# Kernel tuning notes

Hardware: AMD Instinct MI355X
Metric: run time of the kernel (lower is better)

The kernel has to match this reference:

```python
import jax, jax.numpy as jnp
import numpy as np

D_MODEL = 1024
N_HEADS = 16
D_K = D_MODEL // N_HEADS
LN_EPS = 1e-5
NEG = -1e9


def setup_inputs() -> dict:
    key = jax.random.key(0)
    ks = jax.random.split(key, 12)
    B, S = 4, 2048
    s = 1.0 / np.sqrt(D_MODEL)
    # causal mask (1 = keep, 0 = masked)
    causal = jnp.tril(jnp.ones((S, S), dtype=jnp.int32))
    mask = jnp.broadcast_to(causal[None, None], (B, 1, S, S))
    return {
        "Q": jax.random.normal(ks[0], (B, S, D_MODEL), jnp.float32),
        "K": jax.random.normal(ks[1], (B, S, D_MODEL), jnp.float32),
        "V": jax.random.normal(ks[2], (B, S, D_MODEL), jnp.float32),
        "mask": mask,
        "Wq": jax.random.normal(ks[3], (D_MODEL, D_MODEL), jnp.float32) * s,
        "bq": jnp.zeros((D_MODEL,), jnp.float32),
        "Wk": jax.random.normal(ks[4], (D_MODEL, D_MODEL), jnp.float32) * s,
        "bk": jnp.zeros((D_MODEL,), jnp.float32),
        "Wv": jax.random.normal(ks[5], (D_MODEL, D_MODEL), jnp.float32) * s,
        "bv": jnp.zeros((D_MODEL,), jnp.float32),
        "Wo": jax.random.normal(ks[6], (D_MODEL, D_MODEL), jnp.float32) * s,
        "bo": jnp.zeros((D_MODEL,), jnp.float32),
        "ln_gamma": jnp.ones((D_MODEL,), jnp.float32),
        "ln_beta": jnp.zeros((D_MODEL,), jnp.float32),
    }


def _split_heads(x, B, S):
    # (B,S,D) -> (B,H,S,d_k)
    return x.reshape(B, S, N_HEADS, D_K).transpose(0, 2, 1, 3)


def reference(Q, K, V, mask, Wq, bq, Wk, bk, Wv, bv, Wo, bo, ln_gamma, ln_beta):
    B, S, _ = Q.shape
    residual = Q
    q = _split_heads(Q @ Wq + bq, B, S)
    k = _split_heads(K @ Wk + bk, B, S)
    v = _split_heads(V @ Wv + bv, B, S)
    scores = jnp.einsum("bhqd,bhkd->bhqk", q, k) / np.sqrt(D_K).astype(np.float32)
    scores = jnp.where(mask == 0, jnp.float32(NEG), scores)
    attn = jax.nn.softmax(scores, axis=-1)  # dropout p=0 -> identity
    ctx = jnp.einsum("bhqk,bhkd->bhqd", attn, v)
    ctx = ctx.transpose(0, 2, 1, 3).reshape(B, S, D_MODEL)
    out = ctx @ Wo + bo
    x = out + residual
    mu = jnp.mean(x, axis=-1, keepdims=True)
    var = jnp.mean(jnp.square(x - mu), axis=-1, keepdims=True)
    y = (x - mu) * jax.lax.rsqrt(var + LN_EPS) * ln_gamma + ln_beta
    return (y, attn)
```

## Files before the change

kernel.cpp:

```cpp
#include <hip/hip_runtime.h>

#define D_MODEL 1024
#define NH 16
#define DKH 64
#define SEQ 2048
#define BATCH 4
#define ROWS (BATCH*SEQ)

typedef _Float16 f16;
typedef _Float16 f16x4 __attribute__((ext_vector_type(4)));
typedef _Float16 f16x8 __attribute__((ext_vector_type(8)));
typedef float f32x4 __attribute__((ext_vector_type(4)));

#define MFMA16(a,b,c) __builtin_amdgcn_mfma_f32_16x16x32_f16((a),(b),(c),0,0,0)

__device__ __forceinline__ void gload16(const void* g, void* l) {
  __builtin_amdgcn_global_load_lds((const __attribute__((address_space(1))) void*)g,
                                   (__attribute__((address_space(3))) void*)l,
                                   16, 0, 0);
}


__global__ __launch_bounds__(256) void cvt_w_kernel(const float* __restrict__ Wq,
    const float* __restrict__ Wk, const float* __restrict__ Wv, const float* __restrict__ Wo,
    f16* __restrict__ dst)
{
  const float* W = (blockIdx.z==0)?Wq:(blockIdx.z==1)?Wk:(blockIdx.z==2)?Wv:Wo;
  f16* d = dst + (size_t)blockIdx.z * ((size_t)D_MODEL*D_MODEL);
  int idx = blockIdx.x*256 + threadIdx.x;
  int k = idx>>10, n = idx&1023;
  d[(size_t)n*D_MODEL + k] = (f16)W[idx];
}


template<int AF32>
__global__ __launch_bounds__(256) void gemm128(
    const void* __restrict__ A0, const void* __restrict__ A1, const void* __restrict__ A2,
    const f16* __restrict__ WTbase,
    const float* __restrict__ bias0, const float* __restrict__ bias1, const float* __restrict__ bias2,
    f16* __restrict__ out0, f16* __restrict__ out1, f16* __restrict__ out2,
    const float* __restrict__ resid, float* __restrict__ xout, int modeBase)
{
  __shared__ f16 Al[2][128*32];
  __shared__ f16 Bl[2][128*32];
  const int t = threadIdx.x, w = t>>6, l = t&63;
  const int nwg = (int)gridDim.x;
  const int wg = ((int)blockIdx.x & 7) * (nwg >> 3) + ((int)blockIdx.x >> 3);
  const int z  = wg >> 9;
  const int r2 = wg & 511;
  const int bm = r2 >> 3, bn = r2 & 7;
  const int mode = modeBase + z;
  const f16* WT = WTbase + (size_t)mode * ((size_t)D_MODEL*D_MODEL);
  const float* bias = (mode==0)?bias0:(mode==1)?bias1:(mode==2)?bias2:bias0;
  const int wm = w>>1, wn = w&1;
  const int lr = l>>2, lc = l&3, fr = l&15, fg = l>>4;
  f32x4 acc[4][4] = {};
  const char* Bb = (const char*)(WT + (size_t)bn*128*D_MODEL);

#define STAGEB(bufv, ktv) do { \
    char* Bd = (char*)&Bl[0][0] + (bufv)*8192; \
    _Pragma("unroll") \
    for (int cc=0; cc<2; ++cc) { \
      int r0 = w*32 + cc*16; \
      gload16(Bb + (size_t)(r0+lr)*2048 + (ktv)*64 + lc*16, Bd + r0*64); \
    } \
  } while(0)

#define COMPUTEK(bufv) do { \
    const f16* Ac = (const f16*)((char*)&Al[0][0] + (bufv)*8192); \
    const f16* Bc = (const f16*)((char*)&Bl[0][0] + (bufv)*8192); \
    f16x8 a[4], b[4]; \
    _Pragma("unroll") \
    for (int i=0;i<4;++i) a[i] = *(const f16x8*)(Ac + (wm*64+i*16+fr)*32 + fg*8); \
    _Pragma("unroll") \
    for (int j=0;j<4;++j) b[j] = *(const f16x8*)(Bc + (wn*64+j*16+fr)*32 + fg*8); \
    _Pragma("unroll") \
    for (int i=0;i<4;++i) \
      _Pragma("unroll") \
      for (int j=0;j<4;++j) \
        acc[i][j] = MFMA16(a[i], b[j], acc[i][j]); \
  } while(0)

  if constexpr (AF32) {
    const float* A32 = (const float*)((z==0)?A0:(z==1)?A1:A2);
    const float* Arow = A32 + (size_t)(bm*128 + w*32 + (l>>2))*1024 + (l&3)*8;
    f32x4 la[2][2];
    auto LOADA = [&](int ktv) {
      #pragma unroll
      for (int s=0;s<2;++s)
        #pragma unroll
        for (int q=0;q<2;++q)
          la[s][q] = *(const f32x4*)(Arow + (size_t)s*16*1024 + ktv*32 + q*4);
    };
    auto WRITEA = [&](int bufv) {
      char* Ad = (char*)&Al[0][0] + bufv*8192 + w*2048 + l*16;
      #pragma unroll
      for (int s=0;s<2;++s) {
        f16x8 pk;
        #pragma unroll
        for (int q=0;q<2;++q)
          #pragma unroll
          for (int m=0;m<4;++m) pk[q*4+m] = (f16)la[s][q][m];
        *(f16x8*)(Ad + s*1024) = pk;
      }
    };
    LOADA(0); STAGEB(0, 0); WRITEA(0);
    __syncthreads();
    for (int kt=0; kt<31; ++kt) {
      const int cur = kt & 1;
      LOADA(kt+1);
      STAGEB(cur^1, kt+1);
      COMPUTEK(cur);
      WRITEA(cur^1);
      __syncthreads();
    }
    COMPUTEK(1);
  } else {
    const char* Ab = (const char*)((const f16*)A0 + (size_t)bm*128*D_MODEL);
    auto STAGEA = [&](int bufv, int ktv) {
      char* Ad = (char*)&Al[0][0] + bufv*8192;
      #pragma unroll
      for (int cc=0; cc<2; ++cc) {
        int r0 = w*32 + cc*16;
        gload16(Ab + (size_t)(r0+lr)*2048 + ktv*64 + lc*16, Ad + r0*64);
      }
    };
    STAGEA(0,0); STAGEB(0, 0);
    asm volatile("s_waitcnt vmcnt(0)" ::: "memory");
    __builtin_amdgcn_s_barrier();
    for (int kt=0; kt<31; ++kt) {
      const int cur = kt & 1;
      STAGEA(cur^1, kt+1);
      STAGEB(cur^1, kt+1);
      COMPUTEK(cur);
      asm volatile("s_waitcnt vmcnt(0)" ::: "memory");
      __builtin_amdgcn_s_barrier();
    }
    COMPUTEK(1);
  }

#undef STAGEB
#undef COMPUTEK

  #pragma unroll
  for (int j=0;j<4;++j) {
    int col = bn*128 + wn*64 + j*16 + fr;
    float bz = bias[col];
    #pragma unroll
    for (int i=0;i<4;++i) {
      int row0 = bm*128 + wm*64 + i*16 + fg*4;
      f32x4 v = acc[i][j];
      if (mode==0) {
        int hh = col>>6, dk = col&63;
        #pragma unroll
        for (int r=0;r<4;++r) {
          int row = row0+r; int b_ = row>>11, s = row&(SEQ-1);
          out0[((size_t)(b_*NH+hh)*SEQ + s)*DKH + dk] = (f16)((v[r]+bz)*0.125f);
        }
      } else if (mode==1) {
        int hh = col>>6, dk = col&63;
        #pragma unroll
        for (int r=0;r<4;++r) {
          int row = row0+r; int b_ = row>>11, s = row&(SEQ-1);
          out1[((size_t)(b_*NH+hh)*SEQ + s)*DKH + dk] = (f16)(v[r]+bz);
        }
      } else if (mode==2) {
        int hh = col>>6, dk = col&63;
        int b_ = row0>>11, s0 = row0&(SEQ-1);
        f16x4 pk;
        #pragma unroll
        for (int r=0;r<4;++r) pk[r] = (f16)(v[r]+bz);
        *(f16x4*)(out2 + ((size_t)(b_*NH+hh)*DKH + dk)*SEQ + s0) = pk;
      } else {
        #pragma unroll
        for (int r=0;r<4;++r) {
          size_t o = (size_t)(row0+r)*D_MODEL + col;
          xout[o] = v[r] + bz + resid[o];
        }
      }
    }
  }
}


__global__ __launch_bounds__(256) void attn_kernel(
    const f16* __restrict__ qws, const f16* __restrict__ kws, const f16* __restrict__ vTws,
    float* __restrict__ attn, f16* __restrict__ ctx)
{
  __shared__ f16 el[4][32*128];
  const int t = threadIdx.x, w = t>>6, l = t&63;
  const int wg = ((int)blockIdx.x & 7)*128 + ((int)blockIdx.x >> 3);
  const int bh = wg >> 4;
  const int qt = 15 - (wg & 15);
  const int fr = l & 15, fg = l >> 4;
  const f16* qp = qws + ((size_t)bh*SEQ + (size_t)qt*128)*DKH;
  const f16* kp = kws + (size_t)bh*SEQ*DKH;
  const f16* vp = vTws + (size_t)bh*DKH*SEQ;
  float* ap = attn + ((size_t)bh*SEQ + (size_t)qt*128)*SEQ;
  f16* elw = (f16*)&el[w][0];

  for (int kt2 = qt+1; kt2 < 16; ++kt2) {
    f32x4 z4 = {0.f,0.f,0.f,0.f};
    #pragma unroll
    for (int i2=0;i2<16;++i2) {
      int idx = t + i2*256;
      int row = idx >> 5, c4 = idx & 31;
      __builtin_nontemporal_store(z4, (f32x4*)(ap + (size_t)row*SEQ + (size_t)kt2*128 + c4*4));
    }
  }

  f16x8 qf[2][2];
  #pragma unroll
  for (int i=0;i<2;++i)
    #pragma unroll
    for (int kc=0;kc<2;++kc)
      qf[i][kc] = *(const f16x8*)(qp + (w*32 + i*16 + fr)*DKH + kc*32 + fg*8);

  float psum[2] = {0.f, 0.f};
  for (int kt=0; kt<=qt; ++kt) {
    const f16* kb = kp + (size_t)kt*128*DKH;
    const bool diag = (kt == qt);
    #pragma unroll
    for (int jh=0; jh<2; ++jh) {
      f32x4 sc[2][4] = {};
      #pragma unroll
      for (int j2=0;j2<4;++j2) {
        const int j = jh*4 + j2;
        #pragma unroll
        for (int kc=0;kc<2;++kc) {
          f16x8 kf = *(const f16x8*)(kb + (j*16+fr)*DKH + kc*32 + fg*8);
          sc[0][j2] = MFMA16(kf, qf[0][kc], sc[0][j2]);
          sc[1][j2] = MFMA16(kf, qf[1][kc], sc[1][j2]);
        }
      }
      if (diag) {
        #pragma unroll
        for (int i=0;i<2;++i) {
          int rloc = w*32 + i*16 + fr;
          #pragma unroll
          for (int j2=0;j2<4;++j2)
            #pragma unroll
            for (int r=0;r<4;++r) {
              int cloc = (jh*4+j2)*16 + fg*4 + r;
              if (cloc <= rloc) psum[i] += __expf(sc[i][j2][r]);
            }
        }
      } else {
        #pragma unroll
        for (int i=0;i<2;++i)
          #pragma unroll
          for (int j2=0;j2<4;++j2)
            #pragma unroll
            for (int r=0;r<4;++r) psum[i] += __expf(sc[i][j2][r]);
      }
    }
  }
  #pragma unroll
  for (int m=16; m<64; m<<=1) {
    psum[0] += __shfl_xor(psum[0], m, 64);
    psum[1] += __shfl_xor(psum[1], m, 64);
  }
  float rinv[2] = {1.f/psum[0], 1.f/psum[1]};

  f32x4 av[2][4] = {};
  const int swzx = (fr & 7) << 2;
  const int rbrow = l >> 5;
  const int rbslot = l & 31;
  for (int kt=0; kt<=qt; ++kt) {
    const f16* kb = kp + (size_t)kt*128*DKH;
    const bool diag = (kt == qt);
    #pragma unroll
    for (int jh=0; jh<2; ++jh) {
      f32x4 sc[2][4] = {};
      #pragma unroll
      for (int j2=0;j2<4;++j2) {
        const int j = jh*4 + j2;
        #pragma unroll
        for (int kc=0;kc<2;++kc) {
          f16x8 kf = *(const f16x8*)(kb + (j*16+fr)*DKH + kc*32 + fg*8);
          sc[0][j2] = MFMA16(kf, qf[0][kc], sc[0][j2]);
          sc[1][j2] = MFMA16(kf, qf[1][kc], sc[1][j2]);
        }
      }
      #pragma unroll
      for (int i=0;i<2;++i) {
        const int rloc = w*32 + i*16 + fr;
        #pragma unroll
        for (int j2=0;j2<4;++j2) {
          const int j = jh*4 + j2;
          f16x4 ef;
          #pragma unroll
          for (int r=0;r<4;++r) {
            int cloc = j*16 + fg*4 + r;
            float e = (diag && cloc > rloc) ? 0.f : __expf(sc[i][j2][r]) * rinv[i];
            ef[r] = (f16)e;
          }
          *(f16x4*)(elw + (i*16+fr)*128 + (((j*4+fg) ^ swzx) << 2)) = ef;
        }
      }
    }
    {
      float* apk = ap + (size_t)(w*32)*SEQ + (size_t)kt*128;
      #pragma unroll
      for (int p=0;p<16;++p) {
        int row = p*2 + rbrow;
        f16x4 pv4 = *(const f16x4*)(elw + row*128 + ((rbslot ^ ((row&7)<<2)) << 2));
        f32x4 o4; o4[0]=(float)pv4[0]; o4[1]=(float)pv4[1]; o4[2]=(float)pv4[2]; o4[3]=(float)pv4[3];
        __builtin_nontemporal_store(o4, (f32x4*)(apk + (size_t)row*SEQ + rbslot*4));
      }
    }
    #pragma unroll
    for (int c=0;c<4;++c) {
      f16x8 pf0 = *(const f16x8*)(elw + (fr)*128    + (((c*8+fg*2) ^ swzx) << 2));
      f16x8 pf1 = *(const f16x8*)(elw + (16+fr)*128 + (((c*8+fg*2) ^ swzx) << 2));
      #pragma unroll
      for (int j2=0;j2<4;++j2) {
        f16x8 vf = *(const f16x8*)(vp + (j2*16+fr)*SEQ + kt*128 + c*32 + fg*8);
        av[0][j2] = MFMA16(vf, pf0, av[0][j2]);
        av[1][j2] = MFMA16(vf, pf1, av[1][j2]);
      }
    }
  }

  const int b_ = bh >> 4, hh = bh & 15;
  #pragma unroll
  for (int i=0;i<2;++i) {
    size_t rowoff = ((size_t)b_*SEQ + (size_t)qt*128 + w*32 + i*16 + fr) * D_MODEL + hh*DKH;
    #pragma unroll
    for (int j2=0;j2<4;++j2) {
      f16x4 pk;
      #pragma unroll
      for (int r=0;r<4;++r) pk[r] = (f16)av[i][j2][r];
      *(f16x4*)(ctx + rowoff + j2*16 + fg*4) = pk;
    }
  }
}


__global__ __launch_bounds__(256) void ln_kernel(const float* __restrict__ x,
    const float* __restrict__ gamma, const float* __restrict__ beta, float* __restrict__ y)
{
  __shared__ float red[4];
  __shared__ float red2[4];
  const int t = threadIdx.x, w = t>>6, l = t&63;
  const size_t row = blockIdx.x;
  float4 v = ((const float4*)(x + row*D_MODEL))[t];
  float s = v.x+v.y+v.z+v.w;
  #pragma unroll
  for (int m=1;m<64;m<<=1) s += __shfl_xor(s, m, 64);
  if (l==0) red[w] = s;
  __syncthreads();
  float mu = (red[0]+red[1]+red[2]+red[3]) * (1.f/D_MODEL);
  float dx=v.x-mu, dy=v.y-mu, dz=v.z-mu, dw=v.w-mu;
  float q = dx*dx+dy*dy+dz*dz+dw*dw;
  #pragma unroll
  for (int m=1;m<64;m<<=1) q += __shfl_xor(q, m, 64);
  if (l==0) red2[w] = q;
  __syncthreads();
  float var = (red2[0]+red2[1]+red2[2]+red2[3]) * (1.f/D_MODEL);
  float rs = rsqrtf(var + 1e-5f);
  float4 g  = ((const float4*)gamma)[t];
  float4 bb = ((const float4*)beta)[t];
  float4 o;
  o.x = dx*rs*g.x + bb.x;
  o.y = dy*rs*g.y + bb.y;
  o.z = dz*rs*g.z + bb.z;
  o.w = dw*rs*g.w + bb.w;
  ((float4*)(y + row*D_MODEL))[t] = o;
}


extern "C" void kernel_launch(void* const* d_in, const int* in_sizes, int n_in,
                              void* d_out, int out_size, void* d_ws, size_t ws_size,
                              hipStream_t stream)
{
  const float* Q  = (const float*)d_in[0];
  const float* K  = (const float*)d_in[1];
  const float* V  = (const float*)d_in[2];
  const float* Wq = (const float*)d_in[4];
  const float* bq = (const float*)d_in[5];
  const float* Wk = (const float*)d_in[6];
  const float* bk = (const float*)d_in[7];
  const float* Wv = (const float*)d_in[8];
  const float* bv = (const float*)d_in[9];
  const float* Wo = (const float*)d_in[10];
  const float* bo = (const float*)d_in[11];
  const float* gam= (const float*)d_in[12];
  const float* bet= (const float*)d_in[13];

  float* y    = (float*)d_out;
  float* attn = y + (size_t)ROWS*D_MODEL;

  char* ws = (char*)d_ws;
  const size_t SZ = (size_t)ROWS*D_MODEL*sizeof(f16);
  f16* ctx   = (f16*)ws;
  float* xb  = (float*)(ws + SZ);
  f16* WT    = (f16*)(ws + 3*SZ);
  f16* qws   = (f16*)(ws + 3*SZ + ((size_t)4*D_MODEL*D_MODEL*sizeof(f16)));
  f16* kws   = (f16*)((char*)qws + SZ);
  f16* vT    = (f16*)((char*)kws + SZ);

  cvt_w_kernel<<<dim3(4096,1,4), 256, 0, stream>>>(Wq, Wk, Wv, Wo, WT);
  gemm128<1><<<1536, 256, 0, stream>>>(Q, K, V, WT, bq, bk, bv, qws, kws, vT, nullptr, nullptr, 0);
  attn_kernel<<<1024, 256, 0, stream>>>(qws, kws, vT, attn, ctx);
  gemm128<0><<<512, 256, 0, stream>>>(ctx, nullptr, nullptr, WT, bo, bo, bo, nullptr, nullptr, nullptr, Q, xb, 3);
  ln_kernel<<<8192, 256, 0, stream>>>(xb, gam, bet, y);
}
```

Baseline: 502.1 us.

## Warp-specialize attention: dedicated store waves stream attn probabilities from double-buffered LDS

Adds two extra waves per block that write the fp32 attention matrix to global memory, reading from a double-buffered LDS tile that the four compute waves fill one key tile ahead. The upper-triangle zeroing also moves to these store waves, so it runs alongside the softmax normalisation pass. The aim is to overlap the large attn-matrix store traffic with the MFMA work instead of serialising them within each wave. In exchange it doubles LDS use, adds a block barrier per key tile, and changes occupancy through the 384-thread launch bound.

```diff
diff --git a/kernel.cpp b/kernel.cpp
--- a/kernel.cpp
+++ b/kernel.cpp
@@ -183,155 +183,185 @@
 }
 
 
-__global__ __launch_bounds__(256) void attn_kernel(
+#define BAR() do { asm volatile("s_waitcnt lgkmcnt(0)" ::: "memory"); \
+                   __builtin_amdgcn_s_barrier(); } while(0)
+
+__global__ __launch_bounds__(384, 3) void attn_kernel(
     const f16* __restrict__ qws, const f16* __restrict__ kws, const f16* __restrict__ vTws,
     float* __restrict__ attn, f16* __restrict__ ctx)
 {
-  __shared__ f16 el[4][32*128];
+  __shared__ f16 el[2][4][32*128];
   const int t = threadIdx.x, w = t>>6, l = t&63;
   const int wg = ((int)blockIdx.x & 7)*128 + ((int)blockIdx.x >> 3);
   const int bh = wg >> 4;
   const int qt = 15 - (wg & 15);
   const int fr = l & 15, fg = l >> 4;
+  const bool isStore = (w >= 4);
+  const int wc = w & 3;
+  const int ws2 = w - 4;
   const f16* qp = qws + ((size_t)bh*SEQ + (size_t)qt*128)*DKH;
   const f16* kp = kws + (size_t)bh*SEQ*DKH;
   const f16* vp = vTws + (size_t)bh*DKH*SEQ;
   float* ap = attn + ((size_t)bh*SEQ + (size_t)qt*128)*SEQ;
-  f16* elw = (f16*)&el[w][0];
-
-  for (int kt2 = qt+1; kt2 < 16; ++kt2) {
+
+  f16x8 qf[2][2];
+  float psum[2] = {0.f, 0.f};
+  float rinv[2];
+
+  if (!isStore) {
+    #pragma unroll
+    for (int i=0;i<2;++i)
+      #pragma unroll
+      for (int kc=0;kc<2;++kc)
+        qf[i][kc] = *(const f16x8*)(qp + (wc*32 + i*16 + fr)*DKH + kc*32 + fg*8);
+
+    for (int kt=0; kt<=qt; ++kt) {
+      const f16* kb = kp + (size_t)kt*128*DKH;
+      const bool diag = (kt == qt);
+      #pragma unroll
+      for (int jh=0; jh<2; ++jh) {
+        f32x4 sc[2][4] = {};
+        #pragma unroll
+        for (int j2=0;j2<4;++j2) {
+          const int j = jh*4 + j2;
+          #pragma unroll
+          for (int kc=0;kc<2;++kc) {
+            f16x8 kf = *(const f16x8*)(kb + (j*16+fr)*DKH + kc*32 + fg*8);
+            sc[0][j2] = MFMA16(kf, qf[0][kc], sc[0][j2]);
+            sc[1][j2] = MFMA16(kf, qf[1][kc], sc[1][j2]);
+          }
+        }
+        if (diag) {
+          #pragma unroll
+          for (int i=0;i<2;++i) {
+            int rloc = wc*32 + i*16 + fr;
+            #pragma unroll
+            for (int j2=0;j2<4;++j2)
+              #pragma unroll
+              for (int r=0;r<4;++r) {
+                int cloc = (jh*4+j2)*16 + fg*4 + r;
+                if (cloc <= rloc) psum[i] += __expf(sc[i][j2][r]);
+              }
+          }
+        } else {
+          #pragma unroll
+          for (int i=0;i<2;++i)
+            #pragma unroll
+            for (int j2=0;j2<4;++j2)
+              #pragma unroll
+              for (int r=0;r<4;++r) psum[i] += __expf(sc[i][j2][r]);
+        }
+      }
+    }
+    #pragma unroll
+    for (int m=16; m<64; m<<=1) {
+      psum[0] += __shfl_xor(psum[0], m, 64);
+      psum[1] += __shfl_xor(psum[1], m, 64);
+    }
+    rinv[0] = 1.f/psum[0]; rinv[1] = 1.f/psum[1];
+  } else {
+    const int t2 = ws2*64 + l;
     f32x4 z4 = {0.f,0.f,0.f,0.f};
-    #pragma unroll
-    for (int i2=0;i2<16;++i2) {
-      int idx = t + i2*256;
-      int row = idx >> 5, c4 = idx & 31;
-      __builtin_nontemporal_store(z4, (f32x4*)(ap + (size_t)row*SEQ + (size_t)kt2*128 + c4*4));
+    for (int kt2 = qt+1; kt2 < 16; ++kt2) {
+      #pragma unroll 8
+      for (int i2=0;i2<32;++i2) {
+        int idx = t2 + i2*128;
+        int row = idx >> 5, c4 = idx & 31;
+        __builtin_nontemporal_store(z4, (f32x4*)(ap + (size_t)row*SEQ + (size_t)kt2*128 + c4*4));
+      }
     }
   }
 
-  f16x8 qf[2][2];
-  #pragma unroll
-  for (int i=0;i<2;++i)
-    #pragma unroll
-    for (int kc=0;kc<2;++kc)
-      qf[i][kc] = *(const f16x8*)(qp + (w*32 + i*16 + fr)*DKH + kc*32 + fg*8);
-
-  float psum[2] = {0.f, 0.f};
-  for (int kt=0; kt<=qt; ++kt) {
-    const f16* kb = kp + (size_t)kt*128*DKH;
-    const bool diag = (kt == qt);
-    #pragma unroll
-    for (int jh=0; jh<2; ++jh) {
-      f32x4 sc[2][4] = {};
-      #pragma unroll
-      for (int j2=0;j2<4;++j2) {
-        const int j = jh*4 + j2;
-        #pragma unroll
-        for (int kc=0;kc<2;++kc) {
-          f16x8 kf = *(const f16x8*)(kb + (j*16+fr)*DKH + kc*32 + fg*8);
-          sc[0][j2] = MFMA16(kf, qf[0][kc], sc[0][j2]);
-          sc[1][j2] = MFMA16(kf, qf[1][kc], sc[1][j2]);
-        }
-      }
-      if (diag) {
-        #pragma unroll
-        for (int i=0;i<2;++i) {
-          int rloc = w*32 + i*16 + fr;
-          #pragma unroll
-          for (int j2=0;j2<4;++j2)
-            #pragma unroll
-            for (int r=0;r<4;++r) {
-              int cloc = (jh*4+j2)*16 + fg*4 + r;
-              if (cloc <= rloc) psum[i] += __expf(sc[i][j2][r]);
-            }
-        }
-      } else {
-        #pragma unroll
-        for (int i=0;i<2;++i)
-          #pragma unroll
-          for (int j2=0;j2<4;++j2)
-            #pragma unroll
-            for (int r=0;r<4;++r) psum[i] += __expf(sc[i][j2][r]);
-      }
-    }
-  }
-  #pragma unroll
-  for (int m=16; m<64; m<<=1) {
-    psum[0] += __shfl_xor(psum[0], m, 64);
-    psum[1] += __shfl_xor(psum[1], m, 64);
-  }
-  float rinv[2] = {1.f/psum[0], 1.f/psum[1]};
+  BAR();
 
   f32x4 av[2][4] = {};
   const int swzx = (fr & 7) << 2;
   const int rbrow = l >> 5;
   const int rbslot = l & 31;
+
   for (int kt=0; kt<=qt; ++kt) {
-    const f16* kb = kp + (size_t)kt*128*DKH;
-    const bool diag = (kt == qt);
-    #pragma unroll
-    for (int jh=0; jh<2; ++jh) {
-      f32x4 sc[2][4] = {};
-      #pragma unroll
-      for (int j2=0;j2<4;++j2) {
-        const int j = jh*4 + j2;
-        #pragma unroll
-        for (int kc=0;kc<2;++kc) {
-          f16x8 kf = *(const f16x8*)(kb + (j*16+fr)*DKH + kc*32 + fg*8);
-          sc[0][j2] = MFMA16(kf, qf[0][kc], sc[0][j2]);
-          sc[1][j2] = MFMA16(kf, qf[1][kc], sc[1][j2]);
-        }
-      }
-      #pragma unroll
-      for (int i=0;i<2;++i) {
-        const int rloc = w*32 + i*16 + fr;
+    if (!isStore) {
+      f16* elw = &el[kt&1][wc][0];
+      const f16* kb = kp + (size_t)kt*128*DKH;
+      const bool diag = (kt == qt);
+      #pragma unroll
+      for (int jh=0; jh<2; ++jh) {
+        f32x4 sc[2][4] = {};
         #pragma unroll
         for (int j2=0;j2<4;++j2) {
           const int j = jh*4 + j2;
-          f16x4 ef;
-          #pragma unroll
-          for (int r=0;r<4;++r) {
-            int cloc = j*16 + fg*4 + r;
-            float e = (diag && cloc > rloc) ? 0.f : __expf(sc[i][j2][r]) * rinv[i];
-            ef[r] = (f16)e;
+          #pragma unroll
+          for (int kc=0;kc<2;++kc) {
+            f16x8 kf = *(const f16x8*)(kb + (j*16+fr)*DKH + kc*32 + fg*8);
+            sc[0][j2] = MFMA16(kf, qf[0][kc], sc[0][j2]);
+            sc[1][j2] = MFMA16(kf, qf[1][kc], sc[1][j2]);
           }
-          *(f16x4*)(elw + (i*16+fr)*128 + (((j*4+fg) ^ swzx) << 2)) = ef;
-        }
-      }
-    }
-    {
-      float* apk = ap + (size_t)(w*32)*SEQ + (size_t)kt*128;
-      #pragma unroll
-      for (int p=0;p<16;++p) {
-        int row = p*2 + rbrow;
-        f16x4 pv4 = *(const f16x4*)(elw + row*128 + ((rbslot ^ ((row&7)<<2)) << 2));
-        f32x4 o4; o4[0]=(float)pv4[0]; o4[1]=(float)pv4[1]; o4[2]=(float)pv4[2]; o4[3]=(float)pv4[3];
-        __builtin_nontemporal_store(o4, (f32x4*)(apk + (size_t)row*SEQ + rbslot*4));
-      }
-    }
+        }
+        #pragma unroll
+        for (int i=0;i<2;++i) {
+          const int rloc = wc*32 + i*16 + fr;
+          #pragma unroll
+          for (int j2=0;j2<4;++j2) {
+            const int j = jh*4 + j2;
+            f16x4 ef;
+            #pragma unroll
+            for (int r=0;r<4;++r) {
+              int cloc = j*16 + fg*4 + r;
+              float e = (diag && cloc > rloc) ? 0.f : __expf(sc[i][j2][r]) * rinv[i];
+              ef[r] = (f16)e;
+            }
+            *(f16x4*)(elw + (i*16+fr)*128 + (((j*4+fg) ^ swzx) << 2)) = ef;
+          }
+        }
+      }
+      #pragma unroll
+      for (int c=0;c<4;++c) {
+        f16x8 pf0 = *(const f16x8*)(elw + (fr)*128    + (((c*8+fg*2) ^ swzx) << 2));
+        f16x8 pf1 = *(const f16x8*)(elw + (16+fr)*128 + (((c*8+fg*2) ^ swzx) << 2));
+        #pragma unroll
+        for (int j2=0;j2<4;++j2) {
+          f16x8 vf = *(const f16x8*)(vp + (j2*16+fr)*SEQ + kt*128 + c*32 + fg*8);
+          av[0][j2] = MFMA16(vf, pf0, av[0][j2]);
+          av[1][j2] = MFMA16(vf, pf1, av[1][j2]);
+        }
+      }
+    } else if (kt > 0) {
+      const f16* elb = &el[(kt-1)&1][0][0];
+      float* apk = ap + (size_t)(kt-1)*128;
+      #pragma unroll 8
+      for (int p=0;p<32;++p) {
+        int grow = ws2*64 + p*2 + rbrow;
+        const f16* er = elb + (grow>>5)*4096 + (grow&31)*128;
+        f16x4 v4 = *(const f16x4*)(er + ((rbslot ^ ((grow&7)<<2)) << 2));
+        f32x4 o4; o4[0]=(float)v4[0]; o4[1]=(float)v4[1]; o4[2]=(float)v4[2]; o4[3]=(float)v4[3];
+        __builtin_nontemporal_store(o4, (f32x4*)(apk + (size_t)grow*SEQ + rbslot*4));
+      }
+    }
+    BAR();
+  }
+  if (isStore) {
+    const f16* elb = &el[qt&1][0][0];
+    float* apk = ap + (size_t)qt*128;
+    #pragma unroll 8
+    for (int p=0;p<32;++p) {
+      int grow = ws2*64 + p*2 + rbrow;
+      const f16* er = elb + (grow>>5)*4096 + (grow&31)*128;
+      f16x4 v4 = *(const f16x4*)(er + ((rbslot ^ ((grow&7)<<2)) << 2));
+      f32x4 o4; o4[0]=(float)v4[0]; o4[1]=(float)v4[1]; o4[2]=(float)v4[2]; o4[3]=(float)v4[3];
+      __builtin_nontemporal_store(o4, (f32x4*)(apk + (size_t)grow*SEQ + rbslot*4));
+    }
+  } else {
+    const int b_ = bh >> 4, hh = bh & 15;
     #pragma unroll
-    for (int c=0;c<4;++c) {
-      f16x8 pf0 = *(const f16x8*)(elw + (fr)*128    + (((c*8+fg*2) ^ swzx) << 2));
-      f16x8 pf1 = *(const f16x8*)(elw + (16+fr)*128 + (((c*8+fg*2) ^ swzx) << 2));
+    for (int i=0;i<2;++i) {
+      size_t rowoff = ((size_t)b_*SEQ + (size_t)qt*128 + wc*32 + i*16 + fr) * D_MODEL + hh*DKH;
       #pragma unroll
       for (int j2=0;j2<4;++j2) {
-        f16x8 vf = *(const f16x8*)(vp + (j2*16+fr)*SEQ + kt*128 + c*32 + fg*8);
-        av[0][j2] = MFMA16(vf, pf0, av[0][j2]);
-        av[1][j2] = MFMA16(vf, pf1, av[1][j2]);
-      }
-    }
-  }
-
-  const int b_ = bh >> 4, hh = bh & 15;
-  #pragma unroll
-  for (int i=0;i<2;++i) {
-    size_t rowoff = ((size_t)b_*SEQ + (size_t)qt*128 + w*32 + i*16 + fr) * D_MODEL + hh*DKH;
-    #pragma unroll
-    for (int j2=0;j2<4;++j2) {
-      f16x4 pk;
-      #pragma unroll
-      for (int r=0;r<4;++r) pk[r] = (f16)av[i][j2][r];
-      *(f16x4*)(ctx + rowoff + j2*16 + fg*4) = pk;
+        f16x4 pk;
+        #pragma unroll
+        for (int r=0;r<4;++r) pk[r] = (f16)av[i][j2][r];
+        *(f16x4*)(ctx + rowoff + j2*16 + fg*4) = pk;
+      }
     }
   }
 }
@@ -402,7 +432,7 @@
 
   cvt_w_kernel<<<dim3(4096,1,4), 256, 0, stream>>>(Wq, Wk, Wv, Wo, WT);
   gemm128<1><<<1536, 256, 0, stream>>>(Q, K, V, WT, bq, bk, bv, qws, kws, vT, nullptr, nullptr, 0);
-  attn_kernel<<<1024, 256, 0, stream>>>(qws, kws, vT, attn, ctx);
+  attn_kernel<<<1024, 384, 0, stream>>>(qws, kws, vT, attn, ctx);
   gemm128<0><<<512, 256, 0, stream>>>(ctx, nullptr, nullptr, WT, bo, bo, bo, nullptr, nullptr, nullptr, Q, xb, 3);
   ln_kernel<<<8192, 256, 0, stream>>>(xb, gam, bet, y);
 }
```

After: 557.6 us. 11.1% more time.

## Pair complementary causal query tiles per block and interleave zero-fill stores

Applied to the files above, without the earlier changes.

Each attention block now handles two query tiles (qt and 15-qt) for the same batch-head, so every block does the same amount of causal work, and the grid drops from 1024 to 512 blocks. The zero-filling of masked attention tiles is spread across the pass-1 loop with a rate counter, so those stores overlap with compute instead of all being issued at the start. This removes load imbalance and the tail of long blocks. The cost is fewer blocks to hide latency and more registers held for two sets of Q fragments.

```diff
diff --git a/kernel.cpp b/kernel.cpp
--- a/kernel.cpp
+++ b/kernel.cpp
@@ -189,37 +189,44 @@
 {
   __shared__ f16 el[4][32*128];
   const int t = threadIdx.x, w = t>>6, l = t&63;
-  const int wg = ((int)blockIdx.x & 7)*128 + ((int)blockIdx.x >> 3);
-  const int bh = wg >> 4;
-  const int qt = 15 - (wg & 15);
+  const int wg = ((int)blockIdx.x & 7)*64 + ((int)blockIdx.x >> 3);
+  const int bh = wg >> 3;
+  const int pr = wg & 7;
+  const int qtA = pr, qtB = 15 - pr;
   const int fr = l & 15, fg = l >> 4;
-  const f16* qp = qws + ((size_t)bh*SEQ + (size_t)qt*128)*DKH;
   const f16* kp = kws + (size_t)bh*SEQ*DKH;
   const f16* vp = vTws + (size_t)bh*DKH*SEQ;
-  float* ap = attn + ((size_t)bh*SEQ + (size_t)qt*128)*SEQ;
+  const f16* qpA = qws + ((size_t)bh*SEQ + (size_t)qtA*128)*DKH;
+  const f16* qpB = qws + ((size_t)bh*SEQ + (size_t)qtB*128)*DKH;
+  float* apA = attn + ((size_t)bh*SEQ + (size_t)qtA*128)*SEQ;
+  float* apB = attn + ((size_t)bh*SEQ + (size_t)qtB*128)*SEQ;
   f16* elw = (f16*)&el[w][0];
-
-  for (int kt2 = qt+1; kt2 < 16; ++kt2) {
+  const int swzx = (fr & 7) << 2;
+  const int rbrow = l >> 5;
+  const int rbslot = l & 31;
+
+  f16x8 qfA[2][2], qfB[2][2];
+  #pragma unroll
+  for (int i=0;i<2;++i)
+    #pragma unroll
+    for (int kc=0;kc<2;++kc) {
+      qfA[i][kc] = *(const f16x8*)(qpA + (w*32 + i*16 + fr)*DKH + kc*32 + fg*8);
+      qfB[i][kc] = *(const f16x8*)(qpB + (w*32 + i*16 + fr)*DKH + kc*32 + fg*8);
+    }
+
+  auto fill_tile = [&](float* apr, int kt2) {
     f32x4 z4 = {0.f,0.f,0.f,0.f};
     #pragma unroll
     for (int i2=0;i2<16;++i2) {
       int idx = t + i2*256;
       int row = idx >> 5, c4 = idx & 31;
-      __builtin_nontemporal_store(z4, (f32x4*)(ap + (size_t)row*SEQ + (size_t)kt2*128 + c4*4));
-    }
-  }
-
-  f16x8 qf[2][2];
-  #pragma unroll
-  for (int i=0;i<2;++i)
-    #pragma unroll
-    for (int kc=0;kc<2;++kc)
-      qf[i][kc] = *(const f16x8*)(qp + (w*32 + i*16 + fr)*DKH + kc*32 + fg*8);
-
-  float psum[2] = {0.f, 0.f};
-  for (int kt=0; kt<=qt; ++kt) {
-    const f16* kb = kp + (size_t)kt*128*DKH;
-    const bool diag = (kt == qt);
+      __builtin_nontemporal_store(z4, (f32x4*)(apr + (size_t)row*SEQ + (size_t)kt2*128 + c4*4));
+    }
+  };
+  const int cB = pr;
+
+  auto pass1_tile = [&](int ktv, bool diag, const f16x8 (&qf)[2][2], float (&psum)[2]) {
+    const f16* kb = kp + (size_t)ktv*128*DKH;
     #pragma unroll
     for (int jh=0; jh<2; ++jh) {
       f32x4 sc[2][4] = {};
@@ -254,21 +261,33 @@
             for (int r=0;r<4;++r) psum[i] += __expf(sc[i][j2][r]);
       }
     }
+  };
+
+  float psumA[2] = {0.f,0.f}, psumB[2] = {0.f,0.f};
+  int u = 0, f = 0;
+  auto drip_fills = [&]() {
+    while (f*17 < u*15) {
+      if (f < cB) fill_tile(apB, qtB+1+f);
+      else        fill_tile(apA, qtA+1+(f-cB));
+      ++f;
+    }
+  };
+  for (int kt=0; kt<=qtB; ++kt) { pass1_tile(kt, kt==qtB, qfB, psumB); ++u; drip_fills(); }
+  for (int kt=0; kt<=qtA; ++kt) { pass1_tile(kt, kt==qtA, qfA, psumA); ++u; drip_fills(); }
+
+  #pragma unroll
+  for (int m=16; m<64; m<<=1) {
+    psumA[0] += __shfl_xor(psumA[0], m, 64);
+    psumA[1] += __shfl_xor(psumA[1], m, 64);
+    psumB[0] += __shfl_xor(psumB[0], m, 64);
+    psumB[1] += __shfl_xor(psumB[1], m, 64);
   }
-  #pragma unroll
-  for (int m=16; m<64; m<<=1) {
-    psum[0] += __shfl_xor(psum[0], m, 64);
-    psum[1] += __shfl_xor(psum[1], m, 64);
-  }
-  float rinv[2] = {1.f/psum[0], 1.f/psum[1]};
-
-  f32x4 av[2][4] = {};
-  const int swzx = (fr & 7) << 2;
-  const int rbrow = l >> 5;
-  const int rbslot = l & 31;
-  for (int kt=0; kt<=qt; ++kt) {
-    const f16* kb = kp + (size_t)kt*128*DKH;
-    const bool diag = (kt == qt);
+  float rinvA[2] = {1.f/psumA[0], 1.f/psumA[1]};
+  float rinvB[2] = {1.f/psumB[0], 1.f/psumB[1]};
+
+  f32x4 av[2][4];
+  auto pass2_tile = [&](int ktv, bool diag, const f16x8 (&qf)[2][2], const float (&rinv)[2], float* apr) {
+    const f16* kb = kp + (size_t)ktv*128*DKH;
     #pragma unroll
     for (int jh=0; jh<2; ++jh) {
       f32x4 sc[2][4] = {};
@@ -300,7 +319,7 @@
       }
     }
     {
-      float* apk = ap + (size_t)(w*32)*SEQ + (size_t)kt*128;
+      float* apk = apr + (size_t)(w*32)*SEQ + (size_t)ktv*128;
       #pragma unroll
       for (int p=0;p<16;++p) {
         int row = p*2 + rbrow;
@@ -315,25 +334,40 @@
       f16x8 pf1 = *(const f16x8*)(elw + (16+fr)*128 + (((c*8+fg*2) ^ swzx) << 2));
       #pragma unroll
       for (int j2=0;j2<4;++j2) {
-        f16x8 vf = *(const f16x8*)(vp + (j2*16+fr)*SEQ + kt*128 + c*32 + fg*8);
+        f16x8 vf = *(const f16x8*)(vp + (j2*16+fr)*SEQ + ktv*128 + c*32 + fg*8);
         av[0][j2] = MFMA16(vf, pf0, av[0][j2]);
         av[1][j2] = MFMA16(vf, pf1, av[1][j2]);
       }
     }
-  }
-
-  const int b_ = bh >> 4, hh = bh & 15;
-  #pragma unroll
-  for (int i=0;i<2;++i) {
-    size_t rowoff = ((size_t)b_*SEQ + (size_t)qt*128 + w*32 + i*16 + fr) * D_MODEL + hh*DKH;
-    #pragma unroll
-    for (int j2=0;j2<4;++j2) {
-      f16x4 pk;
-      #pragma unroll
-      for (int r=0;r<4;++r) pk[r] = (f16)av[i][j2][r];
-      *(f16x4*)(ctx + rowoff + j2*16 + fg*4) = pk;
-    }
-  }
+  };
+  auto ctx_store = [&](int qtv) {
+    const int b_ = bh >> 4, hh = bh & 15;
+    #pragma unroll
+    for (int i=0;i<2;++i) {
+      size_t rowoff = ((size_t)b_*SEQ + (size_t)qtv*128 + w*32 + i*16 + fr) * D_MODEL + hh*DKH;
+      #pragma unroll
+      for (int j2=0;j2<4;++j2) {
+        f16x4 pk;
+        #pragma unroll
+        for (int r=0;r<4;++r) pk[r] = (f16)av[i][j2][r];
+        *(f16x4*)(ctx + rowoff + j2*16 + fg*4) = pk;
+      }
+    }
+  };
+
+  #pragma unroll
+  for (int i=0;i<2;++i)
+    #pragma unroll
+    for (int j2=0;j2<4;++j2) av[i][j2] = (f32x4){0.f,0.f,0.f,0.f};
+  for (int kt=0; kt<=qtA; ++kt) pass2_tile(kt, kt==qtA, qfA, rinvA, apA);
+  ctx_store(qtA);
+
+  #pragma unroll
+  for (int i=0;i<2;++i)
+    #pragma unroll
+    for (int j2=0;j2<4;++j2) av[i][j2] = (f32x4){0.f,0.f,0.f,0.f};
+  for (int kt=0; kt<=qtB; ++kt) pass2_tile(kt, kt==qtB, qfB, rinvB, apB);
+  ctx_store(qtB);
 }
 
 
@@ -402,7 +436,7 @@
 
   cvt_w_kernel<<<dim3(4096,1,4), 256, 0, stream>>>(Wq, Wk, Wv, Wo, WT);
   gemm128<1><<<1536, 256, 0, stream>>>(Q, K, V, WT, bq, bk, bv, qws, kws, vT, nullptr, nullptr, 0);
-  attn_kernel<<<1024, 256, 0, stream>>>(qws, kws, vT, attn, ctx);
+  attn_kernel<<<512, 256, 0, stream>>>(qws, kws, vT, attn, ctx);
   gemm128<0><<<512, 256, 0, stream>>>(ctx, nullptr, nullptr, WT, bo, bo, bo, nullptr, nullptr, nullptr, Q, xb, 3);
   ln_kernel<<<8192, 256, 0, stream>>>(xb, gam, bet, y);
 }
```

Result: faster. 484.4 us (-3.5%).
